# Kernel optimization log

Hardware: AMD Instinct MI355X
Metric: run time of the kernel (lower is better)

## Reference

```python
import jax, jax.numpy as jnp
import numpy as np

TOP_K = 2

def moe_linear(x, router_w, experts_w):
    # x: [T, din]; router_w: [din, E]; experts_w: [E, din, dout]
    T = x.shape[0]
    E = experts_w.shape[0]
    probs = jax.nn.softmax(x @ router_w, axis=-1)            # [T, E]
    topv, topi = jax.lax.top_k(probs, TOP_K)                 # [T, k]
    topv = topv / jnp.sum(topv, axis=-1, keepdims=True)      # renormalize over selected experts
    w = jnp.zeros((T, E), x.dtype).at[jnp.arange(T)[:, None], topi].set(topv)  # dense routing weights
    y = jnp.zeros((T, experts_w.shape[2]), x.dtype)
    for e in range(E):  # small fixed expert loop; avoids [T,E,dout] intermediate
        y = y + w[:, e:e+1] * (x @ experts_w[e])
    return y

def setup_inputs() -> dict:
    key = jax.random.key(0)
    ks = jax.random.split(key, 7)
    B, S, H, I, E = 4, 2048, 1024, 3584, 8
    sH, sI = 1.0 / np.sqrt(H), 1.0 / np.sqrt(I)
    return {
        "hidden_state": jax.random.normal(ks[0], (B, S, H), jnp.float32),
        "gate_router": jax.random.normal(ks[1], (H, E), jnp.float32) * sH,
        "gate_experts": jax.random.normal(ks[2], (E, H, I), jnp.float32) * sH,
        "up_router": jax.random.normal(ks[3], (H, E), jnp.float32) * sH,
        "up_experts": jax.random.normal(ks[4], (E, H, I), jnp.float32) * sH,
        "down_router": jax.random.normal(ks[5], (I, E), jnp.float32) * sI,
        "down_experts": jax.random.normal(ks[6], (E, I, H), jnp.float32) * sI,
    }

def reference(hidden_state, gate_router, gate_experts, up_router, up_experts, down_router, down_experts):
    B, S, H = hidden_state.shape
    x = hidden_state.reshape(B * S, H)
    g = moe_linear(x, gate_router, gate_experts)             # [T, I]
    u = moe_linear(x, up_router, up_experts)                 # [T, I]
    h = jax.nn.silu(g) * u                                   # SwiGLU
    y = moe_linear(h, down_router, down_experts)             # [T, H]
    return y.reshape(B, S, H)
```

## Files before the change

kernel.cpp:

```cpp
#include <hip/hip_runtime.h>
#include <stdint.h>
#include <stdio.h>

#define T_TOK 8192
#define HDIM  1024
#define IDIM  3584
#define NEXP  8
#define NPAIR (T_TOK*2)
#define BM 128
#define BN 128
#define BK 32

typedef float          f32x4 __attribute__((ext_vector_type(4)));
typedef short          s16x8 __attribute__((ext_vector_type(8)));
typedef unsigned short u16x4 __attribute__((ext_vector_type(4)));
typedef unsigned short u16x8 __attribute__((ext_vector_type(8)));

__device__ __forceinline__ unsigned short f2bf_rne(float f) {
  unsigned u = __float_as_uint(f);
  u += 0x7FFFu + ((u >> 16) & 1u);
  return (unsigned short)(u >> 16);
}
__device__ __forceinline__ float bf2f(unsigned short h) {
  return __uint_as_float(((unsigned)h) << 16);
}

__device__ __forceinline__ void gld16(const void* gsrc, void* ldst) {
  typedef const unsigned int __attribute__((address_space(1))) GU;
  typedef unsigned int       __attribute__((address_space(3))) LU;
  __builtin_amdgcn_global_load_lds((GU*)(unsigned long long)gsrc,
                                   (LU*)(unsigned int)(unsigned long long)ldst,
                                   16, 0, 0);
}

__global__ void split_hilo(const float* __restrict__ in,
                           unsigned short* __restrict__ hi,
                           unsigned short* __restrict__ lo, int n4) {
  int i = blockIdx.x*blockDim.x + threadIdx.x;
  int s = gridDim.x*blockDim.x;
  for (; i < n4; i += s) {
    f32x4 v = ((const f32x4*)in)[i];
    u16x4 h, l;
#pragma unroll
    for (int j = 0; j < 4; j++) {
      float f = v[j];
      unsigned short hb = f2bf_rne(f);
      h[j] = hb;
      l[j] = f2bf_rne(f - bf2f(hb));
    }
    ((u16x4*)hi)[i] = h;
    ((u16x4*)lo)[i] = l;
  }
}

__global__ void transpose_split(const float* __restrict__ W,
                                unsigned short* __restrict__ hi,
                                unsigned short* __restrict__ lo,
                                int K, int N) {
  __shared__ float tile[32][33];
  long base = (long)blockIdx.z * K * N;
  int n0 = blockIdx.x*32, k0 = blockIdx.y*32;
  int tx = threadIdx.x, ty = threadIdx.y;
#pragma unroll
  for (int r = 0; r < 4; r++)
    tile[ty+8*r][tx] = W[base + (long)(k0+ty+8*r)*N + n0 + tx];
  __syncthreads();
#pragma unroll
  for (int r = 0; r < 4; r++) {
    float f = tile[tx][ty+8*r];
    long o = base + (long)(n0+ty+8*r)*K + k0 + tx;
    unsigned short hb = f2bf_rne(f);
    hi[o] = hb;
    if (lo) lo[o] = f2bf_rne(f - bf2f(hb));
  }
}

__global__ void router_topk(const float* __restrict__ X, const float* __restrict__ RW,
                            int K, int* __restrict__ topi, float* __restrict__ topw) {
  int lane = threadIdx.x & 63;
  int t = blockIdx.x*(blockDim.x>>6) + (threadIdx.x>>6);
  if (t >= T_TOK) return;
  const float* xr = X + (long)t*K;
  float acc[NEXP];
#pragma unroll
  for (int e = 0; e < NEXP; e++) acc[e] = 0.f;
  for (int c = lane; c < K; c += 64) {
    float xv = xr[c];
    const float* wr = RW + (long)c*NEXP;
#pragma unroll
    for (int e = 0; e < NEXP; e++) acc[e] += xv*wr[e];
  }
#pragma unroll
  for (int e = 0; e < NEXP; e++) {
    float v = acc[e];
#pragma unroll
    for (int o = 1; o < 64; o <<= 1) v += __shfl_xor(v, o);
    acc[e] = v;
  }
  if (lane == 0) {
    int i0 = 0; float l0 = acc[0];
#pragma unroll
    for (int e = 1; e < NEXP; e++) if (acc[e] > l0) { l0 = acc[e]; i0 = e; }
    int i1 = -1; float l1 = -3.4e38f;
#pragma unroll
    for (int e = 0; e < NEXP; e++) if (e != i0 && acc[e] > l1) { l1 = acc[e]; i1 = e; }
    float w0 = 1.f/(1.f + expf(l1 - l0));
    float w1 = 1.f/(1.f + expf(l0 - l1));
    topi[2*t]   = i0; topi[2*t+1] = i1;
    topw[2*t]   = w0; topw[2*t+1] = w1;
  }
}

__global__ __launch_bounds__(256) void build_perm(const int* __restrict__ topi,
                                                  const float* __restrict__ topw,
                                                  int* __restrict__ offs,
                                                  int* __restrict__ ptok,
                                                  float* __restrict__ pw) {
  int e = blockIdx.x;
  int tid = threadIdx.x, lane = tid & 63, wv = tid >> 6;
  __shared__ int cnt[NEXP];
  __shared__ int wsum[4];
  if (tid < NEXP) cnt[tid] = 0;
  __syncthreads();
  for (int p = tid; p < NPAIR; p += 256) atomicAdd(&cnt[topi[p]], 1);
  __syncthreads();
  int base = 0;
#pragma unroll
  for (int e2 = 0; e2 < NEXP; e2++) if (e2 < e) base += cnt[e2];
  if (tid == 0) { offs[e] = base; if (e == NEXP-1) offs[NEXP] = base + cnt[e]; }
  for (int p0 = 0; p0 < NPAIR; p0 += 256) {
    int p = p0 + tid;
    bool m = (topi[p] == e);
    unsigned long long b = __ballot(m);
    int lp = __popcll(b & ((1ull << lane) - 1ull));
    if (lane == 0) wsum[wv] = __popcll(b);
    __syncthreads();
    int woff = 0;
#pragma unroll
    for (int w2 = 0; w2 < 4; w2++) if (w2 < wv) woff += wsum[w2];
    int tot = wsum[0] + wsum[1] + wsum[2] + wsum[3];
    if (m) { int dst = base + woff + lp; ptok[dst] = p >> 1; pw[dst] = topw[p]; }
    base += tot;
    __syncthreads();
  }
}

__global__ __launch_bounds__(256) void moe_gemm4(
    const unsigned short* __restrict__ Ahi, const unsigned short* __restrict__ Alo,
    const unsigned short* __restrict__ Bhi, const unsigned short* __restrict__ Blo,
    const int* __restrict__ offs, const int* __restrict__ ptok,
    const float* __restrict__ pw, float* __restrict__ out, int K, int N)
{
  const int e = blockIdx.z;
  const int beg = offs[e];
  const int cnt = offs[e+1] - beg;
  const int m0 = blockIdx.y * BM;
  if (m0 >= cnt) return;
  const int n0 = blockIdx.x * BN;

  __shared__ unsigned short Ah[BM*BK], Al[BM*BK], Bh[BN*BK], Bl[BN*BK];
  __shared__ int   stok[BM];
  __shared__ float swt[BM];

  const int tid = threadIdx.x, lane = tid & 63, wv = tid >> 6;
  if (tid < BM) {
    int i = m0 + tid;
    stok[tid] = ptok[beg + (i < cnt ? i : 0)];
    swt[tid]  = (i < cnt) ? pw[beg + i] : 0.f;
  }
  __syncthreads();

  const int srow = lane >> 2;
  const int scol = (lane & 3) * 8;
  const int r0 = (wv*2+0)*16 + srow;
  const int r1 = (wv*2+1)*16 + srow;
  const long a0 = (long)stok[r0]*K + scol;
  const long a1 = (long)stok[r1]*K + scol;
  const long b0 = ((long)e*N + n0 + r0)*K + scol;
  const long b1 = ((long)e*N + n0 + r1)*K + scol;
  unsigned short* dA0  = &Ah[(wv*2+0)*16*BK];
  unsigned short* dA1  = &Ah[(wv*2+1)*16*BK];
  unsigned short* dAl0 = &Al[(wv*2+0)*16*BK];
  unsigned short* dAl1 = &Al[(wv*2+1)*16*BK];
  unsigned short* dB0  = &Bh[(wv*2+0)*16*BK];
  unsigned short* dB1  = &Bh[(wv*2+1)*16*BK];
  unsigned short* dBl0 = &Bl[(wv*2+0)*16*BK];
  unsigned short* dBl1 = &Bl[(wv*2+1)*16*BK];

  f32x4 zero = {0.f, 0.f, 0.f, 0.f};
  f32x4 acc[4][4];
#pragma unroll
  for (int i = 0; i < 4; i++)
#pragma unroll
    for (int j = 0; j < 4; j++) acc[i][j] = zero;

  const int arow = (wv>>1)*64, bcol = (wv&1)*64;
  const int fl = lane & 15, fg = lane >> 4;

  for (int kk = 0; kk < K; kk += BK) {
    __syncthreads();
    gld16(Ahi + a0 + kk, dA0);  gld16(Ahi + a1 + kk, dA1);
    gld16(Alo + a0 + kk, dAl0); gld16(Alo + a1 + kk, dAl1);
    gld16(Bhi + b0 + kk, dB0);  gld16(Bhi + b1 + kk, dB1);
    gld16(Blo + b0 + kk, dBl0); gld16(Blo + b1 + kk, dBl1);
    asm volatile("s_waitcnt vmcnt(0)" ::: "memory");
    __syncthreads();

    s16x8 ahf[4], alf[4], bhf[4], blf[4];
#pragma unroll
    for (int i = 0; i < 4; i++) {
      ahf[i] = *(const s16x8*)&Ah[(arow + i*16 + fl)*BK + fg*8];
      alf[i] = *(const s16x8*)&Al[(arow + i*16 + fl)*BK + fg*8];
      bhf[i] = *(const s16x8*)&Bh[(bcol + i*16 + fl)*BK + fg*8];
      blf[i] = *(const s16x8*)&Bl[(bcol + i*16 + fl)*BK + fg*8];
    }
#pragma unroll
    for (int i = 0; i < 4; i++)
#pragma unroll
      for (int j = 0; j < 4; j++) {
        acc[i][j] = __builtin_amdgcn_mfma_f32_16x16x32_bf16(ahf[i], bhf[j], acc[i][j], 0,0,0);
        acc[i][j] = __builtin_amdgcn_mfma_f32_16x16x32_bf16(alf[i], bhf[j], acc[i][j], 0,0,0);
        acc[i][j] = __builtin_amdgcn_mfma_f32_16x16x32_bf16(ahf[i], blf[j], acc[i][j], 0,0,0);
        acc[i][j] = __builtin_amdgcn_mfma_f32_16x16x32_bf16(alf[i], blf[j], acc[i][j], 0,0,0);
      }
  }

#pragma unroll
  for (int i = 0; i < 4; i++)
#pragma unroll
    for (int r = 0; r < 4; r++) {
      int lrow = arow + i*16 + fg*4 + r;
      if (m0 + lrow < cnt) {
        float wt = swt[lrow];
        long ob = (long)stok[lrow]*N + n0 + bcol + fl;
#pragma unroll
        for (int j = 0; j < 4; j++)
          atomicAdd(&out[ob + j*16], wt * acc[i][j][r]);
      }
    }
}

__global__ void swiglu_k(float* __restrict__ g, const float* __restrict__ u, int n4) {
  int i = blockIdx.x*blockDim.x + threadIdx.x;
  int s = gridDim.x*blockDim.x;
  for (; i < n4; i += s) {
    f32x4 gv = ((const f32x4*)g)[i], uv = ((const f32x4*)u)[i];
#pragma unroll
    for (int j = 0; j < 4; j++) {
      float x = gv[j];
      float sg = 1.f/(1.f + expf(-x));
      gv[j] = x*sg*uv[j];
    }
    ((f32x4*)g)[i] = gv;
  }
}

__global__ __launch_bounds__(256) void moe_gemm_down(
    const float* __restrict__ Hf, const unsigned short* __restrict__ Bw,
    const int* __restrict__ offs, const int* __restrict__ ptok,
    const float* __restrict__ pw, float* __restrict__ out)
{
  const int K = IDIM, N = HDIM;
  const int e = blockIdx.z;
  const int beg = offs[e];
  const int cnt = offs[e+1] - beg;
  const int m0 = blockIdx.y * BM;
  if (m0 >= cnt) return;
  const int n0 = blockIdx.x * BN;

  __shared__ unsigned short Ah[BM*BK], Al[BM*BK], Bh[BN*BK];
  __shared__ int   stok[BM];
  __shared__ float swt[BM];

  const int tid = threadIdx.x, lane = tid & 63, wv = tid >> 6;
  if (tid < BM) {
    int i = m0 + tid;
    stok[tid] = ptok[beg + (i < cnt ? i : 0)];
    swt[tid]  = (i < cnt) ? pw[beg + i] : 0.f;
  }
  __syncthreads();

  const int arw = tid >> 1, half = tid & 1;
  const float* asrc = Hf + (long)stok[arw]*K + half*16;
  unsigned short* awh = &Ah[arw*BK + half*16];
  unsigned short* awl = &Al[arw*BK + half*16];

  const int srow = lane >> 2, scol = (lane & 3)*8;
  const int r0 = (wv*2+0)*16 + srow, r1 = (wv*2+1)*16 + srow;
  const long b0 = ((long)e*N + n0 + r0)*K + scol;
  const long b1 = ((long)e*N + n0 + r1)*K + scol;
  unsigned short* dB0 = &Bh[(wv*2+0)*16*BK];
  unsigned short* dB1 = &Bh[(wv*2+1)*16*BK];

  f32x4 zero = {0.f,0.f,0.f,0.f};
  f32x4 acc[4][4];
#pragma unroll
  for (int i = 0; i < 4; i++)
#pragma unroll
    for (int j = 0; j < 4; j++) acc[i][j] = zero;

  const int arow = (wv>>1)*64, bcol = (wv&1)*64;
  const int fl = lane & 15, fg = lane >> 4;

  for (int kk = 0; kk < K; kk += BK) {
    f32x4 v0 = ((const f32x4*)(asrc + kk))[0];
    f32x4 v1 = ((const f32x4*)(asrc + kk))[1];
    f32x4 v2 = ((const f32x4*)(asrc + kk))[2];
    f32x4 v3 = ((const f32x4*)(asrc + kk))[3];
    u16x8 ha, la, hb2, lb2;
#define SP1(F,HV,LV,IX) { float _f=(F); unsigned short _h=f2bf_rne(_f); HV[IX]=_h; LV[IX]=f2bf_rne(_f - bf2f(_h)); }
    SP1(v0[0],ha,la,0) SP1(v0[1],ha,la,1) SP1(v0[2],ha,la,2) SP1(v0[3],ha,la,3)
    SP1(v1[0],ha,la,4) SP1(v1[1],ha,la,5) SP1(v1[2],ha,la,6) SP1(v1[3],ha,la,7)
    SP1(v2[0],hb2,lb2,0) SP1(v2[1],hb2,lb2,1) SP1(v2[2],hb2,lb2,2) SP1(v2[3],hb2,lb2,3)
    SP1(v3[0],hb2,lb2,4) SP1(v3[1],hb2,lb2,5) SP1(v3[2],hb2,lb2,6) SP1(v3[3],hb2,lb2,7)
#undef SP1
    __syncthreads();
    gld16(Bw + b0 + kk, dB0);
    gld16(Bw + b1 + kk, dB1);
    *(u16x8*)awh = ha;       *(u16x8*)(awh+8) = hb2;
    *(u16x8*)awl = la;       *(u16x8*)(awl+8) = lb2;
    asm volatile("s_waitcnt vmcnt(0)" ::: "memory");
    __syncthreads();

    s16x8 ahf[4], alf[4], bhf[4];
#pragma unroll
    for (int i = 0; i < 4; i++) {
      ahf[i] = *(const s16x8*)&Ah[(arow + i*16 + fl)*BK + fg*8];
      alf[i] = *(const s16x8*)&Al[(arow + i*16 + fl)*BK + fg*8];
      bhf[i] = *(const s16x8*)&Bh[(bcol + i*16 + fl)*BK + fg*8];
    }
#pragma unroll
    for (int i = 0; i < 4; i++)
#pragma unroll
      for (int j = 0; j < 4; j++) {
        acc[i][j] = __builtin_amdgcn_mfma_f32_16x16x32_bf16(ahf[i], bhf[j], acc[i][j], 0,0,0);
        acc[i][j] = __builtin_amdgcn_mfma_f32_16x16x32_bf16(alf[i], bhf[j], acc[i][j], 0,0,0);
      }
  }

#pragma unroll
  for (int i = 0; i < 4; i++)
#pragma unroll
    for (int r = 0; r < 4; r++) {
      int lrow = arow + i*16 + fg*4 + r;
      if (m0 + lrow < cnt) {
        float wt = swt[lrow];
        long ob = (long)stok[lrow]*N + n0 + bcol + fl;
#pragma unroll
        for (int j = 0; j < 4; j++)
          atomicAdd(&out[ob + j*16], wt * acc[i][j][r]);
      }
    }
}

extern "C" void kernel_launch(void* const* d_in, const int* in_sizes, int n_in,
                              void* d_out, int out_size, void* d_ws, size_t ws_size,
                              hipStream_t stream)
{
  (void)in_sizes; (void)n_in;
  const float* x   = (const float*)d_in[0];
  const float* grt = (const float*)d_in[1];
  const float* gex = (const float*)d_in[2];
  const float* urt = (const float*)d_in[3];
  const float* uex = (const float*)d_in[4];
  const float* drt = (const float*)d_in[5];
  const float* dex = (const float*)d_in[6];
  float* out = (float*)d_out;

  char* base = (char*)d_ws;
  size_t off = 0;
  auto alloc = [&](size_t b) -> void* {
    void* r = base + off;
    off = (off + b + 255) & ~(size_t)255;
    return r;
  };
  const size_t szXH = (size_t)T_TOK*HDIM*2;
  const size_t szW  = (size_t)NEXP*HDIM*IDIM*2;
  const size_t szGI = (size_t)T_TOK*IDIM*4;

  unsigned short* xhi   = (unsigned short*)alloc(szXH);
  unsigned short* xlo   = (unsigned short*)alloc(szXH);
  unsigned short* wg_hi = (unsigned short*)alloc(szW);
  unsigned short* wg_lo = (unsigned short*)alloc(szW);
  unsigned short* wu_hi = (unsigned short*)alloc(szW);
  unsigned short* wu_lo = (unsigned short*)alloc(szW);
  float* gbuf = (float*)alloc(szGI);
  int*   topi_g = (int*)alloc(NPAIR*4);  float* topw_g = (float*)alloc(NPAIR*4);
  int*   topi_u = (int*)alloc(NPAIR*4);  float* topw_u = (float*)alloc(NPAIR*4);
  int*   topi_d = (int*)alloc(NPAIR*4);  float* topw_d = (float*)alloc(NPAIR*4);
  int* offs_g = (int*)alloc(64);
  int* offs_u = (int*)alloc(64);
  int* offs_d = (int*)alloc(64);
  int*   ptok_g = (int*)alloc(NPAIR*4);  float* pw_g = (float*)alloc(NPAIR*4);
  int*   ptok_u = (int*)alloc(NPAIR*4);  float* pw_u = (float*)alloc(NPAIR*4);
  int*   ptok_d = (int*)alloc(NPAIR*4);  float* pw_d = (float*)alloc(NPAIR*4);

  float*          ubuf  = (float*)wg_hi;
  unsigned short* wd_hi = wu_hi;

  if (off > ws_size) {
    fprintf(stderr, "[moe] ws too small: need %zu bytes, have %zu\n", off, ws_size);
    hipMemsetAsync(d_out, 0, (size_t)out_size*sizeof(float), stream);
    return;
  }

  hipMemsetAsync(gbuf, 0, szGI, stream);
  hipMemsetAsync(d_out, 0, (size_t)out_size*sizeof(float), stream);

  split_hilo<<<2048, 256, 0, stream>>>(x, xhi, xlo, T_TOK*HDIM/4);
  transpose_split<<<dim3(IDIM/32, HDIM/32, NEXP), dim3(32,8), 0, stream>>>(gex, wg_hi, wg_lo, HDIM, IDIM);
  transpose_split<<<dim3(IDIM/32, HDIM/32, NEXP), dim3(32,8), 0, stream>>>(uex, wu_hi, wu_lo, HDIM, IDIM);
  router_topk<<<T_TOK/4, 256, 0, stream>>>(x, grt, HDIM, topi_g, topw_g);
  router_topk<<<T_TOK/4, 256, 0, stream>>>(x, urt, HDIM, topi_u, topw_u);
  build_perm<<<NEXP, 256, 0, stream>>>(topi_g, topw_g, offs_g, ptok_g, pw_g);
  build_perm<<<NEXP, 256, 0, stream>>>(topi_u, topw_u, offs_u, ptok_u, pw_u);

  moe_gemm4<<<dim3(IDIM/BN, T_TOK/BM, NEXP), 256, 0, stream>>>(
      xhi, xlo, wg_hi, wg_lo, offs_g, ptok_g, pw_g, gbuf, HDIM, IDIM);

  hipMemsetAsync(ubuf, 0, szGI, stream);
  moe_gemm4<<<dim3(IDIM/BN, T_TOK/BM, NEXP), 256, 0, stream>>>(
      xhi, xlo, wu_hi, wu_lo, offs_u, ptok_u, pw_u, ubuf, HDIM, IDIM);

  transpose_split<<<dim3(HDIM/32, IDIM/32, NEXP), dim3(32,8), 0, stream>>>(dex, wd_hi, nullptr, IDIM, HDIM);

  swiglu_k<<<2048, 256, 0, stream>>>(gbuf, ubuf, T_TOK*IDIM/4);

  router_topk<<<T_TOK/4, 256, 0, stream>>>(gbuf, drt, IDIM, topi_d, topw_d);
  build_perm<<<NEXP, 256, 0, stream>>>(topi_d, topw_d, offs_d, ptok_d, pw_d);

  moe_gemm_down<<<dim3(HDIM/BN, T_TOK/BM, NEXP), 256, 0, stream>>>(
      gbuf, wd_hi, offs_d, ptok_d, pw_d, out);
}
```

Baseline: 1.817 ms.

## Double-buffer MoE GEMM tiles, swizzle block order, fuse routers and SwiGLU

Adds LDS double buffering to both grouped MoE GEMMs so the next K-tile's global loads (and the down-projection's hi/lo conversion) overlap the current tile's MFMA work. It also remaps block indices with an 8-way swizzle to change L2 locality. The gate and up routers are merged into one kernel, and the down router is folded into the SwiGLU pass, which removes extra reads of the activations. Doubled LDS use may lower occupancy, and the swizzle assumes the block count divides by 8.

Result: slower. 4.530 ms (+149.4%).

```diff
diff --git a/kernel.cpp b/kernel.cpp
--- a/kernel.cpp
+++ b/kernel.cpp
@@ -75,40 +75,52 @@
   }
 }
 
-__global__ void router_topk(const float* __restrict__ X, const float* __restrict__ RW,
-                            int K, int* __restrict__ topi, float* __restrict__ topw) {
+__device__ __forceinline__ void top2_write(const float* acc, int t,
+                                           int* __restrict__ topi,
+                                           float* __restrict__ topw) {
+  int i0 = 0; float l0 = acc[0];
+#pragma unroll
+  for (int e = 1; e < NEXP; e++) if (acc[e] > l0) { l0 = acc[e]; i0 = e; }
+  int i1 = -1; float l1 = -3.4e38f;
+#pragma unroll
+  for (int e = 0; e < NEXP; e++) if (e != i0 && acc[e] > l1) { l1 = acc[e]; i1 = e; }
+  float w0 = 1.f/(1.f + expf(l1 - l0));
+  float w1 = 1.f/(1.f + expf(l0 - l1));
+  topi[2*t]   = i0; topi[2*t+1] = i1;
+  topw[2*t]   = w0; topw[2*t+1] = w1;
+}
+
+__global__ __launch_bounds__(256) void router2_topk(
+    const float* __restrict__ X,
+    const float* __restrict__ RWg, const float* __restrict__ RWu,
+    int* __restrict__ tig, float* __restrict__ twg,
+    int* __restrict__ tiu, float* __restrict__ twu) {
   int lane = threadIdx.x & 63;
-  int t = blockIdx.x*(blockDim.x>>6) + (threadIdx.x>>6);
-  if (t >= T_TOK) return;
-  const float* xr = X + (long)t*K;
-  float acc[NEXP];
-#pragma unroll
-  for (int e = 0; e < NEXP; e++) acc[e] = 0.f;
-  for (int c = lane; c < K; c += 64) {
-    float xv = xr[c];
-    const float* wr = RW + (long)c*NEXP;
-#pragma unroll
-    for (int e = 0; e < NEXP; e++) acc[e] += xv*wr[e];
+  int t = blockIdx.x*4 + (threadIdx.x>>6);
+  const f32x4* xr = (const f32x4*)(X + (long)t*HDIM);
+  float ag[NEXP], au[NEXP];
+#pragma unroll
+  for (int e = 0; e < NEXP; e++) { ag[e] = 0.f; au[e] = 0.f; }
+#pragma unroll
+  for (int it = 0; it < HDIM/4/64; it++) {
+    int c4 = it*64 + lane;
+    f32x4 xv = xr[c4];
+#pragma unroll
+    for (int j = 0; j < 4; j++) {
+      const float* wg = RWg + (long)(c4*4+j)*NEXP;
+      const float* wu = RWu + (long)(c4*4+j)*NEXP;
+#pragma unroll
+      for (int e = 0; e < NEXP; e++) { ag[e] += xv[j]*wg[e]; au[e] += xv[j]*wu[e]; }
+    }
   }
 #pragma unroll
   for (int e = 0; e < NEXP; e++) {
-    float v = acc[e];
-#pragma unroll
-    for (int o = 1; o < 64; o <<= 1) v += __shfl_xor(v, o);
-    acc[e] = v;
-  }
-  if (lane == 0) {
-    int i0 = 0; float l0 = acc[0];
-#pragma unroll
-    for (int e = 1; e < NEXP; e++) if (acc[e] > l0) { l0 = acc[e]; i0 = e; }
-    int i1 = -1; float l1 = -3.4e38f;
-#pragma unroll
-    for (int e = 0; e < NEXP; e++) if (e != i0 && acc[e] > l1) { l1 = acc[e]; i1 = e; }
-    float w0 = 1.f/(1.f + expf(l1 - l0));
-    float w1 = 1.f/(1.f + expf(l0 - l1));
-    topi[2*t]   = i0; topi[2*t+1] = i1;
-    topw[2*t]   = w0; topw[2*t+1] = w1;
-  }
+    float vg = ag[e], vu = au[e];
+#pragma unroll
+    for (int o = 1; o < 64; o <<= 1) { vg += __shfl_xor(vg, o); vu += __shfl_xor(vu, o); }
+    ag[e] = vg; au[e] = vu;
+  }
+  if (lane == 0) { top2_write(ag, t, tig, twg); top2_write(au, t, tiu, twu); }
 }
 
 __global__ __launch_bounds__(256) void build_perm(const int* __restrict__ topi,
@@ -154,11 +166,14 @@
   const int e = blockIdx.z;
   const int beg = offs[e];
   const int cnt = offs[e+1] - beg;
-  const int m0 = blockIdx.y * BM;
+  const int nwg = gridDim.x * gridDim.y;
+  const int orig = blockIdx.y * gridDim.x + blockIdx.x;
+  const int swz = (orig & 7) * (nwg >> 3) + (orig >> 3);
+  const int m0 = (swz / gridDim.x) * BM;
   if (m0 >= cnt) return;
-  const int n0 = blockIdx.x * BN;
-
-  __shared__ unsigned short Ah[BM*BK], Al[BM*BK], Bh[BN*BK], Bl[BN*BK];
+  const int n0 = (swz % gridDim.x) * BN;
+
+  __shared__ unsigned short Ah[2][BM*BK], Al[2][BM*BK], Bh[2][BN*BK], Bl[2][BN*BK];
   __shared__ int   stok[BM];
   __shared__ float swt[BM];
 
@@ -178,14 +193,19 @@
   const long a1 = (long)stok[r1]*K + scol;
   const long b0 = ((long)e*N + n0 + r0)*K + scol;
   const long b1 = ((long)e*N + n0 + r1)*K + scol;
-  unsigned short* dA0  = &Ah[(wv*2+0)*16*BK];
-  unsigned short* dA1  = &Ah[(wv*2+1)*16*BK];
-  unsigned short* dAl0 = &Al[(wv*2+0)*16*BK];
-  unsigned short* dAl1 = &Al[(wv*2+1)*16*BK];
-  unsigned short* dB0  = &Bh[(wv*2+0)*16*BK];
-  unsigned short* dB1  = &Bh[(wv*2+1)*16*BK];
-  unsigned short* dBl0 = &Bl[(wv*2+0)*16*BK];
-  unsigned short* dBl1 = &Bl[(wv*2+1)*16*BK];
+  const int o0 = (wv*2+0)*16*BK;
+  const int o1 = (wv*2+1)*16*BK;
+
+#define STAGE4(buf, kk) do {                                     \
+    gld16(Ahi + a0 + (kk), &Ah[buf][o0]);                        \
+    gld16(Ahi + a1 + (kk), &Ah[buf][o1]);                        \
+    gld16(Alo + a0 + (kk), &Al[buf][o0]);                        \
+    gld16(Alo + a1 + (kk), &Al[buf][o1]);                        \
+    gld16(Bhi + b0 + (kk), &Bh[buf][o0]);                        \
+    gld16(Bhi + b1 + (kk), &Bh[buf][o1]);                        \
+    gld16(Blo + b0 + (kk), &Bl[buf][o0]);                        \
+    gld16(Blo + b1 + (kk), &Bl[buf][o1]);                        \
+  } while (0)
 
   f32x4 zero = {0.f, 0.f, 0.f, 0.f};
   f32x4 acc[4][4];
@@ -197,22 +217,21 @@
   const int arow = (wv>>1)*64, bcol = (wv&1)*64;
   const int fl = lane & 15, fg = lane >> 4;
 
+  STAGE4(0, 0);
+  asm volatile("s_waitcnt vmcnt(0)" ::: "memory");
+  __syncthreads();
+
+  int cur = 0;
   for (int kk = 0; kk < K; kk += BK) {
-    __syncthreads();
-    gld16(Ahi + a0 + kk, dA0);  gld16(Ahi + a1 + kk, dA1);
-    gld16(Alo + a0 + kk, dAl0); gld16(Alo + a1 + kk, dAl1);
-    gld16(Bhi + b0 + kk, dB0);  gld16(Bhi + b1 + kk, dB1);
-    gld16(Blo + b0 + kk, dBl0); gld16(Blo + b1 + kk, dBl1);
-    asm volatile("s_waitcnt vmcnt(0)" ::: "memory");
-    __syncthreads();
+    if (kk + BK < K) STAGE4(cur^1, kk + BK);
 
     s16x8 ahf[4], alf[4], bhf[4], blf[4];
 #pragma unroll
     for (int i = 0; i < 4; i++) {
-      ahf[i] = *(const s16x8*)&Ah[(arow + i*16 + fl)*BK + fg*8];
-      alf[i] = *(const s16x8*)&Al[(arow + i*16 + fl)*BK + fg*8];
-      bhf[i] = *(const s16x8*)&Bh[(bcol + i*16 + fl)*BK + fg*8];
-      blf[i] = *(const s16x8*)&Bl[(bcol + i*16 + fl)*BK + fg*8];
+      ahf[i] = *(const s16x8*)&Ah[cur][(arow + i*16 + fl)*BK + fg*8];
+      alf[i] = *(const s16x8*)&Al[cur][(arow + i*16 + fl)*BK + fg*8];
+      bhf[i] = *(const s16x8*)&Bh[cur][(bcol + i*16 + fl)*BK + fg*8];
+      blf[i] = *(const s16x8*)&Bl[cur][(bcol + i*16 + fl)*BK + fg*8];
     }
 #pragma unroll
     for (int i = 0; i < 4; i++)
@@ -223,7 +242,12 @@
         acc[i][j] = __builtin_amdgcn_mfma_f32_16x16x32_bf16(ahf[i], blf[j], acc[i][j], 0,0,0);
         acc[i][j] = __builtin_amdgcn_mfma_f32_16x16x32_bf16(alf[i], blf[j], acc[i][j], 0,0,0);
       }
-  }
+
+    asm volatile("s_waitcnt vmcnt(0)" ::: "memory");
+    __syncthreads();
+    cur ^= 1;
+  }
+#undef STAGE4
 
 #pragma unroll
   for (int i = 0; i < 4; i++)
@@ -240,19 +264,42 @@
     }
 }
 
-__global__ void swiglu_k(float* __restrict__ g, const float* __restrict__ u, int n4) {
-  int i = blockIdx.x*blockDim.x + threadIdx.x;
-  int s = gridDim.x*blockDim.x;
-  for (; i < n4; i += s) {
-    f32x4 gv = ((const f32x4*)g)[i], uv = ((const f32x4*)u)[i];
+__global__ __launch_bounds__(256) void swiglu_router(
+    float* __restrict__ g, const float* __restrict__ u,
+    const float* __restrict__ RW,
+    int* __restrict__ topi, float* __restrict__ topw) {
+  int lane = threadIdx.x & 63;
+  int t = blockIdx.x*4 + (threadIdx.x>>6);
+  f32x4*       gr = (f32x4*)(g + (long)t*IDIM);
+  const f32x4* ur = (const f32x4*)(u + (long)t*IDIM);
+  float acc[NEXP];
+#pragma unroll
+  for (int e = 0; e < NEXP; e++) acc[e] = 0.f;
+#pragma unroll
+  for (int it = 0; it < IDIM/4/64; it++) {
+    int c4 = it*64 + lane;
+    f32x4 gv = gr[c4], uv = ur[c4], hv;
 #pragma unroll
     for (int j = 0; j < 4; j++) {
       float x = gv[j];
-      float sg = 1.f/(1.f + expf(-x));
-      gv[j] = x*sg*uv[j];
-    }
-    ((f32x4*)g)[i] = gv;
-  }
+      hv[j] = x * uv[j] / (1.f + expf(-x));
+    }
+    gr[c4] = hv;
+#pragma unroll
+    for (int j = 0; j < 4; j++) {
+      const float* wr = RW + (long)(c4*4+j)*NEXP;
+#pragma unroll
+      for (int e = 0; e < NEXP; e++) acc[e] += hv[j]*wr[e];
+    }
+  }
+#pragma unroll
+  for (int e = 0; e < NEXP; e++) {
+    float v = acc[e];
+#pragma unroll
+    for (int o = 1; o < 64; o <<= 1) v += __shfl_xor(v, o);
+    acc[e] = v;
+  }
+  if (lane == 0) top2_write(acc, t, topi, topw);
 }
 
 __global__ __launch_bounds__(256) void moe_gemm_down(
@@ -264,11 +311,14 @@
   const int e = blockIdx.z;
   const int beg = offs[e];
   const int cnt = offs[e+1] - beg;
-  const int m0 = blockIdx.y * BM;
+  const int nwg = gridDim.x * gridDim.y;
+  const int orig = blockIdx.y * gridDim.x + blockIdx.x;
+  const int swz = (orig & 7) * (nwg >> 3) + (orig >> 3);
+  const int m0 = (swz / gridDim.x) * BM;
   if (m0 >= cnt) return;
-  const int n0 = blockIdx.x * BN;
-
-  __shared__ unsigned short Ah[BM*BK], Al[BM*BK], Bh[BN*BK];
+  const int n0 = (swz % gridDim.x) * BN;
+
+  __shared__ unsigned short Ah[2][BM*BK], Al[2][BM*BK], Bh[2][BN*BK];
   __shared__ int   stok[BM];
   __shared__ float swt[BM];
 
@@ -282,15 +332,36 @@
 
   const int arw = tid >> 1, half = tid & 1;
   const float* asrc = Hf + (long)stok[arw]*K + half*16;
-  unsigned short* awh = &Ah[arw*BK + half*16];
-  unsigned short* awl = &Al[arw*BK + half*16];
+  const int awoff = arw*BK + half*16;
 
   const int srow = lane >> 2, scol = (lane & 3)*8;
   const int r0 = (wv*2+0)*16 + srow, r1 = (wv*2+1)*16 + srow;
   const long b0 = ((long)e*N + n0 + r0)*K + scol;
   const long b1 = ((long)e*N + n0 + r1)*K + scol;
-  unsigned short* dB0 = &Bh[(wv*2+0)*16*BK];
-  unsigned short* dB1 = &Bh[(wv*2+1)*16*BK];
+  const int o0 = (wv*2+0)*16*BK, o1 = (wv*2+1)*16*BK;
+
+  f32x4 p0, p1, p2, p3;
+  u16x8 ha, la, hb2, lb2;
+
+#define LOADA(kk) do {                        \
+    p0 = ((const f32x4*)(asrc + (kk)))[0];    \
+    p1 = ((const f32x4*)(asrc + (kk)))[1];    \
+    p2 = ((const f32x4*)(asrc + (kk)))[2];    \
+    p3 = ((const f32x4*)(asrc + (kk)))[3];    \
+  } while (0)
+#define SP1(F,HV,LV,IX) { float _f=(F); unsigned short _h=f2bf_rne(_f); HV[IX]=_h; LV[IX]=f2bf_rne(_f - bf2f(_h)); }
+#define CVTWR(buf) do {                                                   \
+    SP1(p0[0],ha,la,0) SP1(p0[1],ha,la,1) SP1(p0[2],ha,la,2) SP1(p0[3],ha,la,3) \
+    SP1(p1[0],ha,la,4) SP1(p1[1],ha,la,5) SP1(p1[2],ha,la,6) SP1(p1[3],ha,la,7) \
+    SP1(p2[0],hb2,lb2,0) SP1(p2[1],hb2,lb2,1) SP1(p2[2],hb2,lb2,2) SP1(p2[3],hb2,lb2,3) \
+    SP1(p3[0],hb2,lb2,4) SP1(p3[1],hb2,lb2,5) SP1(p3[2],hb2,lb2,6) SP1(p3[3],hb2,lb2,7) \
+    *(u16x8*)&Ah[buf][awoff]     = ha;  *(u16x8*)&Ah[buf][awoff+8] = hb2; \
+    *(u16x8*)&Al[buf][awoff]     = la;  *(u16x8*)&Al[buf][awoff+8] = lb2; \
+  } while (0)
+#define STAGEB(buf, kk) do {                  \
+    gld16(Bw + b0 + (kk), &Bh[buf][o0]);      \
+    gld16(Bw + b1 + (kk), &Bh[buf][o1]);      \
+  } while (0)
 
   f32x4 zero = {0.f,0.f,0.f,0.f};
   f32x4 acc[4][4];
@@ -302,32 +373,23 @@
   const int arow = (wv>>1)*64, bcol = (wv&1)*64;
   const int fl = lane & 15, fg = lane >> 4;
 
+  LOADA(0);
+  STAGEB(0, 0);
+  CVTWR(0);
+  asm volatile("s_waitcnt vmcnt(0)" ::: "memory");
+  __syncthreads();
+
+  int cur = 0;
   for (int kk = 0; kk < K; kk += BK) {
-    f32x4 v0 = ((const f32x4*)(asrc + kk))[0];
-    f32x4 v1 = ((const f32x4*)(asrc + kk))[1];
-    f32x4 v2 = ((const f32x4*)(asrc + kk))[2];
-    f32x4 v3 = ((const f32x4*)(asrc + kk))[3];
-    u16x8 ha, la, hb2, lb2;
-#define SP1(F,HV,LV,IX) { float _f=(F); unsigned short _h=f2bf_rne(_f); HV[IX]=_h; LV[IX]=f2bf_rne(_f - bf2f(_h)); }
-    SP1(v0[0],ha,la,0) SP1(v0[1],ha,la,1) SP1(v0[2],ha,la,2) SP1(v0[3],ha,la,3)
-    SP1(v1[0],ha,la,4) SP1(v1[1],ha,la,5) SP1(v1[2],ha,la,6) SP1(v1[3],ha,la,7)
-    SP1(v2[0],hb2,lb2,0) SP1(v2[1],hb2,lb2,1) SP1(v2[2],hb2,lb2,2) SP1(v2[3],hb2,lb2,3)
-    SP1(v3[0],hb2,lb2,4) SP1(v3[1],hb2,lb2,5) SP1(v3[2],hb2,lb2,6) SP1(v3[3],hb2,lb2,7)
-#undef SP1
-    __syncthreads();
-    gld16(Bw + b0 + kk, dB0);
-    gld16(Bw + b1 + kk, dB1);
-    *(u16x8*)awh = ha;       *(u16x8*)(awh+8) = hb2;
-    *(u16x8*)awl = la;       *(u16x8*)(awl+8) = lb2;
-    asm volatile("s_waitcnt vmcnt(0)" ::: "memory");
-    __syncthreads();
+    const bool nx = (kk + BK < K);
+    if (nx) { LOADA(kk + BK); STAGEB(cur^1, kk + BK); }
 
     s16x8 ahf[4], alf[4], bhf[4];
 #pragma unroll
     for (int i = 0; i < 4; i++) {
-      ahf[i] = *(const s16x8*)&Ah[(arow + i*16 + fl)*BK + fg*8];
-      alf[i] = *(const s16x8*)&Al[(arow + i*16 + fl)*BK + fg*8];
-      bhf[i] = *(const s16x8*)&Bh[(bcol + i*16 + fl)*BK + fg*8];
+      ahf[i] = *(const s16x8*)&Ah[cur][(arow + i*16 + fl)*BK + fg*8];
+      alf[i] = *(const s16x8*)&Al[cur][(arow + i*16 + fl)*BK + fg*8];
+      bhf[i] = *(const s16x8*)&Bh[cur][(bcol + i*16 + fl)*BK + fg*8];
     }
 #pragma unroll
     for (int i = 0; i < 4; i++)
@@ -336,7 +398,16 @@
         acc[i][j] = __builtin_amdgcn_mfma_f32_16x16x32_bf16(ahf[i], bhf[j], acc[i][j], 0,0,0);
         acc[i][j] = __builtin_amdgcn_mfma_f32_16x16x32_bf16(alf[i], bhf[j], acc[i][j], 0,0,0);
       }
-  }
+
+    if (nx) CVTWR(cur^1);
+    asm volatile("s_waitcnt vmcnt(0)" ::: "memory");
+    __syncthreads();
+    cur ^= 1;
+  }
+#undef LOADA
+#undef SP1
+#undef CVTWR
+#undef STAGEB
 
 #pragma unroll
   for (int i = 0; i < 4; i++)
@@ -410,8 +481,7 @@
   split_hilo<<<2048, 256, 0, stream>>>(x, xhi, xlo, T_TOK*HDIM/4);
   transpose_split<<<dim3(IDIM/32, HDIM/32, NEXP), dim3(32,8), 0, stream>>>(gex, wg_hi, wg_lo, HDIM, IDIM);
   transpose_split<<<dim3(IDIM/32, HDIM/32, NEXP), dim3(32,8), 0, stream>>>(uex, wu_hi, wu_lo, HDIM, IDIM);
-  router_topk<<<T_TOK/4, 256, 0, stream>>>(x, grt, HDIM, topi_g, topw_g);
-  router_topk<<<T_TOK/4, 256, 0, stream>>>(x, urt, HDIM, topi_u, topw_u);
+  router2_topk<<<T_TOK/4, 256, 0, stream>>>(x, grt, urt, topi_g, topw_g, topi_u, topw_u);
   build_perm<<<NEXP, 256, 0, stream>>>(topi_g, topw_g, offs_g, ptok_g, pw_g);
   build_perm<<<NEXP, 256, 0, stream>>>(topi_u, topw_u, offs_u, ptok_u, pw_u);
 
@@ -424,9 +494,7 @@
 
   transpose_split<<<dim3(HDIM/32, IDIM/32, NEXP), dim3(32,8), 0, stream>>>(dex, wd_hi, nullptr, IDIM, HDIM);
 
-  swiglu_k<<<2048, 256, 0, stream>>>(gbuf, ubuf, T_TOK*IDIM/4);
-
-  router_topk<<<T_TOK/4, 256, 0, stream>>>(gbuf, drt, IDIM, topi_d, topw_d);
+  swiglu_router<<<T_TOK/4, 256, 0, stream>>>(gbuf, ubuf, drt, topi_d, topw_d);
   build_perm<<<NEXP, 256, 0, stream>>>(topi_d, topw_d, offs_d, ptok_d, pw_d);
 
   moe_gemm_down<<<dim3(HDIM/BN, T_TOK/BM, NEXP), 256, 0, stream>>>(
```
